# Performance work log

Hardware: AMD Instinct MI355X
Metric: run time of the kernel (lower is better)

Reference implementation:

```python
import jax, jax.numpy as jnp
import numpy as np

# Grid / filter configuration (matches init_kwargs)
NLAT_IN, NLON_IN = 361, 720
NLAT_OUT, NLON_OUT = 361, 720
K = 9                       # kernel_size for piecewise-linear basis, kernel_shape=[3,4]
PSCALE = NLON_IN // NLON_OUT  # longitude stride between output longitudes
NNZ = 65536
B, CIN, COUT = 2, 64, 64


def setup_inputs() -> dict:
    key = jax.random.key(0)
    k0, k1, k2, k3, k4, k5 = jax.random.split(key, 6)
    x = jax.random.normal(k0, (B, CIN, NLAT_IN, NLON_IN), dtype=jnp.float32)
    psi_ker_idx = jax.random.randint(k1, (NNZ,), 0, K)
    psi_row_idx = jax.random.randint(k2, (NNZ,), 0, NLAT_OUT)
    psi_col_idx = jax.random.randint(k3, (NNZ,), 0, NLAT_IN * NLON_IN)
    # quadrature-merged, normalized basis values are small positive numbers
    psi_vals = jax.random.uniform(k4, (NNZ,), dtype=jnp.float32) / K
    scale = (1.0 / (CIN * K)) ** 0.5
    weight = scale * jax.random.normal(k5, (COUT, CIN, K), dtype=jnp.float32)
    bias = jnp.zeros((COUT,), dtype=jnp.float32)
    return {
        "x": x,
        "psi_vals": psi_vals,
        "weight": weight,
        "bias": bias,
        "psi_ker_idx": psi_ker_idx,
        "psi_row_idx": psi_row_idx,
        "psi_col_idx": psi_col_idx,
    }


def reference(x, psi_vals, weight, bias, psi_ker_idx, psi_row_idx, psi_col_idx):
    """DISCO S2 conv: y[b,c,k,lo,p] = sum_nz psi_vals * x[b,c,lat_in, (lon_in+p*PSCALE)%NLON_IN]
    restricted to nz with ker==k, row==lo; then channel mixing with weight (COUT,CIN,K) + bias.
    Matches torch fallback which rolls x by PSCALE per output longitude and does sparse bmm."""
    b, c, nlat_in, nlon_in = x.shape
    lat_in = psi_col_idx // nlon_in          # (nnz,)
    lon_in = psi_col_idx % nlon_in           # (nnz,)
    seg = psi_ker_idx * NLAT_OUT + psi_row_idx  # (nnz,) segment id over (K, nlat_out)
    xf = x.reshape(b * c, nlat_in, nlon_in)

    def step(carry, p):
        lon = (lon_in + p * PSCALE) % nlon_in        # rolled longitude index, (nnz,)
        g = xf[:, lat_in, lon]                       # (BC, nnz) gather
        contrib = (psi_vals * g).T                   # (nnz, BC)
        yk = jax.ops.segment_sum(contrib, seg, num_segments=K * NLAT_OUT)  # (K*nlat_out, BC)
        y = yk.reshape(K, NLAT_OUT, b, c)
        o = jnp.einsum("klbc,ock->bol", y, weight)   # (B, COUT, nlat_out)
        return carry, o

    _, ys = jax.lax.scan(step, None, jnp.arange(NLON_OUT))  # (nlon_out, B, COUT, nlat_out)
    out = jnp.moveaxis(ys, 0, -1)                            # (B, COUT, nlat_out, nlon_out)
    return out + bias[None, :, None, None]
```

## Files before the change

### kernel.cpp

```cpp
#include <hip/hip_runtime.h>

typedef unsigned int uint;
typedef unsigned short ushort;

#define NLAT 361
#define NLON 720
#define NNZT 65536
#define CIN 64
#define COUT 64
#define NK 9
#define PADL 784
#define ROWCAP 384
#define CKTOT 576
#define YPS 168
#define WTS 640

typedef __attribute__((ext_vector_type(8))) short short8v;
typedef __attribute__((ext_vector_type(4))) float f32x4;

__device__ __forceinline__ float bfu(uint u){ return __uint_as_float(u<<16); }
__device__ __forceinline__ float bfh(uint u){ return __uint_as_float(u & 0xffff0000u); }
__device__ __forceinline__ ushort f2bf(float f){
  uint b = __float_as_uint(f);
  return (ushort)((b + 0x7fffu + ((b>>16)&1u)) >> 16);
}
__device__ __forceinline__ uint packbf2(float f0, float f1){
  uint b0 = __float_as_uint(f0), b1 = __float_as_uint(f1);
  uint r0 = (b0 + 0x7fffu + ((b0>>16)&1u)) >> 16;
  uint r1 = ((b1 + 0x7fffu + ((b1>>16)&1u)) >> 16) << 16;
  return r0 | r1;
}

__global__ __launch_bounds__(256) void k_csr(const int* __restrict__ ker, const int* __restrict__ row,
                                             const int* __restrict__ col, const float* __restrict__ vals,
                                             int2* __restrict__ meta_g, int* __restrict__ kptr_g){
  const int lo = blockIdx.x, tid = threadIdx.x;
  __shared__ int cnt2[256*NK];
  #pragma unroll
  for (int kk=0;kk<NK;kk++) cnt2[tid*NK+kk]=0;
  __syncthreads();
  for (int i=tid;i<NNZT;i+=256) if (row[i]==lo) cnt2[tid*NK + ker[i]]++;
  __syncthreads();
  if (tid==0){
    int run=0;
    for (int kk=0;kk<NK;kk++){
      kptr_g[lo*10+kk]=run;
      for (int t=0;t<256;t++){ int tmp=cnt2[t*NK+kk]; cnt2[t*NK+kk]=run; run+=tmp; }
    }
    kptr_g[lo*10+9]=run;
  }
  __syncthreads();
  for (int i=tid;i<NNZT;i+=256) if (row[i]==lo){
    int kk=ker[i];
    int off=cnt2[tid*NK+kk]++;
    if (off<ROWCAP){
      int c=col[i];
      meta_g[lo*ROWCAP+off]=make_int2(((c/NLON)<<16)|(c%NLON), __float_as_int(vals[i]));
    }
  }
}

__global__ __launch_bounds__(256) void k_xb(const float* __restrict__ x, ushort* __restrict__ xb){
  const int bid=blockIdx.x, tid=threadIdx.x;
  const int b=bid/NLAT, lat=bid-b*NLAT;
  const float* xs = x + (size_t)b*CIN*NLAT*NLON + (size_t)lat*NLON;
  ushort* xd = xb + (size_t)(b*NLAT+lat)*16*PADL*4;
  const size_t S=(size_t)NLAT*NLON;
  for (int idx=tid; idx<16*PADL; idx+=256){
    int cq=idx/PADL, j=idx-cq*PADL;
    int jj = (j<NLON)? j : j-NLON;
    const float* xc = xs + (size_t)(cq*4)*S + jj;
    uint lo32 = packbf2(xc[0], xc[S]);
    uint hi32 = packbf2(xc[2*S], xc[3*S]);
    *(uint2*)(xd + (size_t)(cq*PADL + j)*4) = make_uint2(lo32, hi32);
  }
}

__global__ __launch_bounds__(256) void k_wt(const float* __restrict__ w, ushort* __restrict__ wt){
  int idx = blockIdx.x*256 + threadIdx.x;
  if (idx >= COUT*WTS) return;
  int oc = idx/WTS, ckl = idx-oc*WTS;
  int chunk = ckl/160, q = ckl-chunk*160;
  ushort v = 0;
  if (q < 144) v = f2bf(w[oc*CKTOT + chunk*144 + q]);
  wt[oc*WTS + ckl] = v;
}

template<int USE_XB>
__global__ __launch_bounds__(256,3) void k_main(const float* __restrict__ x, const ushort* __restrict__ xb,
    const int2* __restrict__ meta_g, const int* __restrict__ kptr_g,
    const ushort* __restrict__ wt, const float* __restrict__ bias, float* __restrict__ out){
  const int bid=blockIdx.x, tid=threadIdx.x;
  const int lo=bid/6; const int rem=bid-lo*6;
  const int b=rem/3, pq=rem-(rem/3)*3;

  __shared__ int2 meta[ROWCAP];
  __shared__ __align__(16) ushort Yp[64*YPS];

  int kp[10];
  #pragma unroll
  for (int kk=0;kk<10;kk++){ int v=kptr_g[lo*10+kk]; kp[kk]=v<ROWCAP?v:ROWCAP; }
  for (int i=tid;i<kp[9];i+=256) meta[i]=meta_g[lo*ROWCAP+i];
  for (int idx=tid; idx<64*8; idx+=256){
    int p=idx>>3, j=idx&7;
    *(uint*)((char*)Yp + p*(YPS*2) + 288 + j*4) = 0;
  }
  __syncthreads();

  const int lane=tid&63, wv=tid>>6;
  const int l15=lane&15, kg=lane>>4;
  const char* xb8 = (const char*)xb + (size_t)b*NLAT*16*PADL*8;
  const char* wtb = (const char*)wt + ((wv*16+l15)*WTS + kg*8)*2;
  const char* ypb = (const char*)Yp + l15*(YPS*2) + kg*16;

  float b4[4];
  #pragma unroll
  for (int r=0;r<4;r++) b4[r]=bias[wv*16 + kg*4 + r];

  f32x4 outacc[4][4];
  #pragma unroll
  for (int a=0;a<4;a++)
    #pragma unroll
    for (int c2=0;c2<4;c2++) outacc[a][c2]=(f32x4)0.f;

  for (int chunk=0;chunk<4;chunk++){
    const int c0=chunk*16;
    short8v af[5];
    #pragma unroll
    for (int ks=0;ks<5;ks++)
      af[ks] = *(const short8v*)(wtb + (chunk*160 + ks*32)*2);

    const uint cqoff = (uint)(chunk*4+wv)*(PADL*8);
    #pragma unroll
    for (int pt=0;pt<4;pt++){
      const int p0 = pq*240 + pt*64;
      float acc[4][NK];
      #pragma unroll
      for (int j=0;j<4;j++)
        #pragma unroll
        for (int kk=0;kk<NK;kk++) acc[j][kk]=0.f;

#define GBODY(M,KK) { \
      int lat=(M).x>>16, lon=(M).x&0xffff; \
      float v=__int_as_float((M).y); \
      int s=lon+p0; s=(s>=NLON)?s-NLON:s; \
      uint off=(uint)lat*(16u*PADL*8u)+cqoff+(uint)(s+lane)*8u; \
      uint2 u=*(const uint2*)(xb8+off); \
      acc[0][KK]+=v*bfu(u.x); acc[1][KK]+=v*bfh(u.x); \
      acc[2][KK]+=v*bfu(u.y); acc[3][KK]+=v*bfh(u.y); }

#define GBODYF(M,KK) { \
      int lat=(M).x>>16, lon=(M).x&0xffff; \
      float v=__int_as_float((M).y); \
      int s=lon+p0; s=(s>=NLON)?s-NLON:s; \
      int widx=s+lane; widx=(widx>=NLON)?widx-NLON:widx; \
      int base=((b*CIN + c0+wv*4)*NLAT + lat)*NLON + widx; \
      acc[0][KK]+=v*x[base]; \
      acc[1][KK]+=v*x[base+NLAT*NLON]; \
      acc[2][KK]+=v*x[base+2*NLAT*NLON]; \
      acc[3][KK]+=v*x[base+3*NLAT*NLON]; }

      #pragma unroll
      for (int kk=0;kk<NK;kk++){
        int i=kp[kk]; const int e=kp[kk+1];
        if (USE_XB){
          for (; i+3<e; i+=4){
            int2 m0=meta[i], m1=meta[i+1], m2=meta[i+2], m3=meta[i+3];
            GBODY(m0,kk); GBODY(m1,kk); GBODY(m2,kk); GBODY(m3,kk);
          }
          for (; i<e; i++){ int2 m0=meta[i]; GBODY(m0,kk); }
        } else {
          for (; i<e; i++){ int2 m0=meta[i]; GBODYF(m0,kk); }
        }
      }
#undef GBODY
#undef GBODYF
      __syncthreads();
      {
        char* dst = (char*)Yp + lane*(YPS*2) + wv*72;
        #pragma unroll
        for (int i2=0;i2<18;i2++){
          const int t0=2*i2, t1=2*i2+1;
          uint pr = packbf2(acc[t0/9][t0-9*(t0/9)], acc[t1/9][t1-9*(t1/9)]);
          *(uint*)(dst + i2*4) = pr;
        }
      }
      __syncthreads();
      #pragma unroll
      for (int ptile=0;ptile<4;ptile++){
        #pragma unroll
        for (int ks=0;ks<5;ks++){
          short8v bf = *(const short8v*)(ypb + ptile*(16*YPS*2) + ks*64);
          outacc[pt][ptile] = __builtin_amdgcn_mfma_f32_16x16x32_bf16(af[ks], bf, outacc[pt][ptile], 0, 0, 0);
        }
      }
    }
  }
  #pragma unroll
  for (int pt=0;pt<4;pt++)
    #pragma unroll
    for (int ptile=0;ptile<4;ptile++){
      const int pidx = pt*64 + ptile*16;
      if (pidx < 240){
        #pragma unroll
        for (int r=0;r<4;r++){
          int oc = wv*16 + kg*4 + r;
          int p  = pq*240 + pidx + l15;
          out[((size_t)(b*COUT+oc)*NLAT + lo)*NLON + p] = outacc[pt][ptile][r] + b4[r];
        }
      }
    }
}

extern "C" void kernel_launch(void* const* d_in, const int* in_sizes, int n_in,
                              void* d_out, int out_size, void* d_ws, size_t ws_size,
                              hipStream_t stream){
  const float* x   =(const float*)d_in[0];
  const float* vals=(const float*)d_in[1];
  const float* w   =(const float*)d_in[2];
  const float* bias=(const float*)d_in[3];
  const int* ker=(const int*)d_in[4];
  const int* row=(const int*)d_in[5];
  const int* col=(const int*)d_in[6];
  float* out=(float*)d_out;

  const size_t META_B=(size_t)NLAT*ROWCAP*sizeof(int2);
  const size_t KPTR_B=((size_t)NLAT*10*sizeof(int)+15)&~(size_t)15;
  const size_t WT_B=((size_t)COUT*WTS*sizeof(ushort)+15)&~(size_t)15;
  const size_t XB_B=(size_t)2*NLAT*16*PADL*4*sizeof(ushort);
  int2* meta_g=(int2*)d_ws;
  int*  kptr_g=(int*)((char*)d_ws+META_B);
  ushort* wt=(ushort*)((char*)d_ws+META_B+KPTR_B);
  ushort* xb=(ushort*)((char*)d_ws+META_B+KPTR_B+WT_B);
  const bool use_xb = ws_size >= META_B+KPTR_B+WT_B+XB_B;

  k_csr<<<dim3(NLAT), dim3(256), 0, stream>>>(ker,row,col,vals,meta_g,kptr_g);
  k_wt <<<dim3((COUT*WTS+255)/256), dim3(256), 0, stream>>>(w, wt);
  if (use_xb){
    k_xb<<<dim3(2*NLAT), dim3(256), 0, stream>>>(x, xb);
    k_main<1><<<dim3(NLAT*6), dim3(256), 0, stream>>>(x,xb,meta_g,kptr_g,wt,bias,out);
  } else {
    k_main<0><<<dim3(NLAT*6), dim3(256), 0, stream>>>(x,xb,meta_g,kptr_g,wt,bias,out);
  }
}
```

Baseline: 2.045 ms.

## Restructure DISCO main kernel: per-wave kernel-slot split, sorted nnz, cooperative grid sync

The main kernel is rebuilt so each block handles one (output latitude, batch) pair and covers all longitudes in three passes. Each wave now takes a balanced subset of the kernel-basis indices and accumulates 16 channels at once, instead of splitting channels across waves. The CSR build sorts nonzeros by gather address and packs value, kernel index and longitude into one word, with value precision truncated. A cooperative launch with grid-wide syncs keeps blocks in lockstep over channel chunks to improve L2 reuse of the bf16 input. The cost is grid-sync overhead, extra per-block setup work, and lower precision in psi values.

New measurement: 2.260 ms. 10.5% more time.

```diff
diff --git a/kernel.cpp b/kernel.cpp
--- a/kernel.cpp
+++ b/kernel.cpp
@@ -1,4 +1,5 @@
 #include <hip/hip_runtime.h>
+#include <hip/hip_cooperative_groups.h>
 
 typedef unsigned int uint;
 typedef unsigned short ushort;
@@ -14,6 +15,9 @@
 #define CKTOT 576
 #define YPS 168
 #define WTS 640
+#define XROWB (16*PADL*8)
+#define GRIDC 722
+#define OCAP 128
 
 typedef __attribute__((ext_vector_type(8))) short short8v;
 typedef __attribute__((ext_vector_type(4))) float f32x4;
@@ -35,29 +39,40 @@
                                              const int* __restrict__ col, const float* __restrict__ vals,
                                              int2* __restrict__ meta_g, int* __restrict__ kptr_g){
   const int lo = blockIdx.x, tid = threadIdx.x;
-  __shared__ int cnt2[256*NK];
-  #pragma unroll
-  for (int kk=0;kk<NK;kk++) cnt2[tid*NK+kk]=0;
-  __syncthreads();
-  for (int i=tid;i<NNZT;i+=256) if (row[i]==lo) cnt2[tid*NK + ker[i]]++;
-  __syncthreads();
-  if (tid==0){
-    int run=0;
-    for (int kk=0;kk<NK;kk++){
-      kptr_g[lo*10+kk]=run;
-      for (int t=0;t<256;t++){ int tmp=cnt2[t*NK+kk]; cnt2[t*NK+kk]=run; run+=tmp; }
-    }
-    kptr_g[lo*10+9]=run;
-  }
-  __syncthreads();
+  __shared__ int cnt[256];
+  __shared__ int2 list[ROWCAP];
+  __shared__ int kc[NK];
+  __shared__ int ntot;
+  int c=0;
+  for (int i=tid;i<NNZT;i+=256) if (row[i]==lo) c++;
+  cnt[tid]=c;
+  if (tid<NK) kc[tid]=0;
+  __syncthreads();
+  if (tid==0){ int run=0; for (int t=0;t<256;t++){ int tmp=cnt[t]; cnt[t]=run; run+=tmp; } ntot=run; }
+  __syncthreads();
+  int off=cnt[tid];
   for (int i=tid;i<NNZT;i+=256) if (row[i]==lo){
-    int kk=ker[i];
-    int off=cnt2[tid*NK+kk]++;
     if (off<ROWCAP){
-      int c=col[i];
-      meta_g[lo*ROWCAP+off]=make_int2(((c/NLON)<<16)|(c%NLON), __float_as_int(vals[i]));
-    }
-  }
+      int cc=col[i]; int lat=cc/NLON, lon=cc-lat*NLON;
+      int kk=ker[i];
+      uint vb=__float_as_uint(vals[i])&0xffffc000u;
+      list[off]=make_int2(lat*XROWB+lon*8, (int)(vb|((uint)kk<<10)|(uint)lon));
+      atomicAdd(&kc[kk],1);
+    }
+    off++;
+  }
+  __syncthreads();
+  int n = ntot; if (n>ROWCAP) n=ROWCAP;
+  for (int i=tid;i<n;i+=256){
+    uint xi=(uint)list[i].x; int r=0;
+    for (int j=0;j<n;j++){
+      uint xj=(uint)list[j].x;
+      r += (xj<xi) || (xj==xi && j<i);
+    }
+    meta_g[lo*ROWCAP+r]=list[i];
+  }
+  if (tid<NK) kptr_g[lo*10+tid]=kc[tid];
+  if (tid==NK) kptr_g[lo*10+9]=n;
 }
 
 __global__ __launch_bounds__(256) void k_xb(const float* __restrict__ x, ushort* __restrict__ xb){
@@ -82,134 +97,171 @@
   int oc = idx/WTS, ckl = idx-oc*WTS;
   int chunk = ckl/160, q = ckl-chunk*160;
   ushort v = 0;
-  if (q < 144) v = f2bf(w[oc*CKTOT + chunk*144 + q]);
+  if (q < 144){
+    int wvq=q/36, r=q-wvq*36;
+    int kk=r>>2, j=r&3;
+    v = f2bf(w[oc*CKTOT + (chunk*16 + wvq*4 + j)*NK + kk]);
+  }
   wt[oc*WTS + ckl] = v;
 }
 
-template<int USE_XB>
-__global__ __launch_bounds__(256,3) void k_main(const float* __restrict__ x, const ushort* __restrict__ xb,
+template<int USE_XB, int SYNC>
+__global__ __launch_bounds__(256,3) void k_coop(const float* __restrict__ x, const ushort* __restrict__ xb,
     const int2* __restrict__ meta_g, const int* __restrict__ kptr_g,
     const ushort* __restrict__ wt, const float* __restrict__ bias, float* __restrict__ out){
-  const int bid=blockIdx.x, tid=threadIdx.x;
-  const int lo=bid/6; const int rem=bid-lo*6;
-  const int b=rem/3, pq=rem-(rem/3)*3;
+  const int wid=blockIdx.x, tid=threadIdx.x;
+  const int lane=tid&63, wv=tid>>6, l15=lane&15, kg=lane>>4;
+  const int lo=wid>>1, b=wid&1;
 
   __shared__ int2 meta[ROWCAP];
   __shared__ __align__(16) ushort Yp[64*YPS];
-
-  int kp[10];
-  #pragma unroll
-  for (int kk=0;kk<10;kk++){ int v=kptr_g[lo*10+kk]; kp[kk]=v<ROWCAP?v:ROWCAP; }
-  for (int i=tid;i<kp[9];i+=256) meta[i]=meta_g[lo*ROWCAP+i];
+  __shared__ ushort olist[4*OCAP];
+
+  int n = kptr_g[lo*10+9]; if (n>ROWCAP) n=ROWCAP;
+  for (int i=tid;i<n;i+=256) meta[i]=meta_g[lo*ROWCAP+i];
+  int kbase, klen;
+  {
+    int P[10]; P[0]=0;
+    #pragma unroll
+    for (int k=0;k<9;k++) P[k+1]=P[k]+kptr_g[lo*10+k];
+    const int Bn[4][5]={{0,3,5,7,9},{0,2,5,7,9},{0,2,4,7,9},{0,2,4,6,9}};
+    int best=1<<30, br=0;
+    #pragma unroll
+    for (int r=0;r<4;r++){
+      int m0=P[Bn[r][1]]-P[0], m1=P[Bn[r][2]]-P[Bn[r][1]];
+      int m2=P[Bn[r][3]]-P[Bn[r][2]], m3=P[9]-P[Bn[r][3]];
+      int mx=max(max(m0,m1),max(m2,m3));
+      if (mx<best){best=mx;br=r;}
+    }
+    kbase=Bn[br][wv]; klen=Bn[br][wv+1]-Bn[br][wv];
+  }
   for (int idx=tid; idx<64*8; idx+=256){
     int p=idx>>3, j=idx&7;
-    *(uint*)((char*)Yp + p*(YPS*2) + 288 + j*4) = 0;
-  }
-  __syncthreads();
-
-  const int lane=tid&63, wv=tid>>6;
-  const int l15=lane&15, kg=lane>>4;
-  const char* xb8 = (const char*)xb + (size_t)b*NLAT*16*PADL*8;
+    *(uint*)((char*)Yp + p*(YPS*2) + 288 + j*4)=0;
+  }
+  __syncthreads();
+  int ocount=0;
+  for (int i=0;i<n;i++){
+    int k=(int)(((uint)meta[i].y>>10)&15u);
+    if ((unsigned)(k-kbase)<(unsigned)klen && ocount<OCAP){
+      if (lane==0) olist[wv*OCAP+ocount]=(ushort)i;
+      ocount++;
+    }
+  }
+  __syncthreads();
+
+  const char* xb8 = (const char*)xb + (size_t)b*NLAT*(size_t)XROWB;
   const char* wtb = (const char*)wt + ((wv*16+l15)*WTS + kg*8)*2;
   const char* ypb = (const char*)Yp + l15*(YPS*2) + kg*16;
-
-  float b4[4];
+  char* ydst = (char*)Yp + lane*(YPS*2);
+  const ushort* ol = &olist[wv*OCAP];
+  const int SS = NLAT*NLON;
+
+#define C16(S) { \
+  acc[0][0][S]+=v*bfu(u0.x); acc[0][1][S]+=v*bfh(u0.x); acc[0][2][S]+=v*bfu(u0.y); acc[0][3][S]+=v*bfh(u0.y); \
+  acc[1][0][S]+=v*bfu(u1.x); acc[1][1][S]+=v*bfh(u1.x); acc[1][2][S]+=v*bfu(u1.y); acc[1][3][S]+=v*bfh(u1.y); \
+  acc[2][0][S]+=v*bfu(u2.x); acc[2][1][S]+=v*bfh(u2.x); acc[2][2][S]+=v*bfu(u2.y); acc[2][3][S]+=v*bfh(u2.y); \
+  acc[3][0][S]+=v*bfu(u3.x); acc[3][1][S]+=v*bfh(u3.x); acc[3][2][S]+=v*bfu(u3.y); acc[3][3][S]+=v*bfh(u3.y); }
+#define C16F(S) { \
+  acc[0][0][S]+=v*x[fb]; acc[0][1][S]+=v*x[fb+SS]; acc[0][2][S]+=v*x[fb+2*SS]; acc[0][3][S]+=v*x[fb+3*SS]; \
+  acc[1][0][S]+=v*x[fb+4*SS]; acc[1][1][S]+=v*x[fb+5*SS]; acc[1][2][S]+=v*x[fb+6*SS]; acc[1][3][S]+=v*x[fb+7*SS]; \
+  acc[2][0][S]+=v*x[fb+8*SS]; acc[2][1][S]+=v*x[fb+9*SS]; acc[2][2][S]+=v*x[fb+10*SS]; acc[2][3][S]+=v*x[fb+11*SS]; \
+  acc[3][0][S]+=v*x[fb+12*SS]; acc[3][1][S]+=v*x[fb+13*SS]; acc[3][2][S]+=v*x[fb+14*SS]; acc[3][3][S]+=v*x[fb+15*SS]; }
+
+  f32x4 outacc[3][4];
   #pragma unroll
-  for (int r=0;r<4;r++) b4[r]=bias[wv*16 + kg*4 + r];
-
-  f32x4 outacc[4][4];
-  #pragma unroll
-  for (int a=0;a<4;a++)
+  for (int a=0;a<3;a++)
     #pragma unroll
     for (int c2=0;c2<4;c2++) outacc[a][c2]=(f32x4)0.f;
 
-  for (int chunk=0;chunk<4;chunk++){
-    const int c0=chunk*16;
-    short8v af[5];
-    #pragma unroll
-    for (int ks=0;ks<5;ks++)
-      af[ks] = *(const short8v*)(wtb + (chunk*160 + ks*32)*2);
-
-    const uint cqoff = (uint)(chunk*4+wv)*(PADL*8);
-    #pragma unroll
-    for (int pt=0;pt<4;pt++){
-      const int p0 = pq*240 + pt*64;
-      float acc[4][NK];
-      #pragma unroll
-      for (int j=0;j<4;j++)
+  for (int pt=0;pt<4;pt++){
+    for (int chunk=0;chunk<4;chunk++){
+      if constexpr (SYNC) cooperative_groups::this_grid().sync();
+      const char* xq0 = xb8 + (size_t)(chunk*4+0)*(PADL*8);
+      const char* xq1 = xb8 + (size_t)(chunk*4+1)*(PADL*8);
+      const char* xq2 = xb8 + (size_t)(chunk*4+2)*(PADL*8);
+      const char* xq3 = xb8 + (size_t)(chunk*4+3)*(PADL*8);
+      for (int it=0;it<3;it++){
+        const int p0 = it*240 + pt*64;
+        const uint thr = (uint)(NLON-p0);
+        const uint lanep8 = (uint)(lane+p0)*8u;
+        const bool act = (pt<3) || (lane<48);
+        const int jmax = act ? ocount : 0;
+        float acc[4][4][3];
         #pragma unroll
-        for (int kk=0;kk<NK;kk++) acc[j][kk]=0.f;
-
-#define GBODY(M,KK) { \
-      int lat=(M).x>>16, lon=(M).x&0xffff; \
-      float v=__int_as_float((M).y); \
-      int s=lon+p0; s=(s>=NLON)?s-NLON:s; \
-      uint off=(uint)lat*(16u*PADL*8u)+cqoff+(uint)(s+lane)*8u; \
-      uint2 u=*(const uint2*)(xb8+off); \
-      acc[0][KK]+=v*bfu(u.x); acc[1][KK]+=v*bfh(u.x); \
-      acc[2][KK]+=v*bfu(u.y); acc[3][KK]+=v*bfh(u.y); }
-
-#define GBODYF(M,KK) { \
-      int lat=(M).x>>16, lon=(M).x&0xffff; \
-      float v=__int_as_float((M).y); \
-      int s=lon+p0; s=(s>=NLON)?s-NLON:s; \
-      int widx=s+lane; widx=(widx>=NLON)?widx-NLON:widx; \
-      int base=((b*CIN + c0+wv*4)*NLAT + lat)*NLON + widx; \
-      acc[0][KK]+=v*x[base]; \
-      acc[1][KK]+=v*x[base+NLAT*NLON]; \
-      acc[2][KK]+=v*x[base+2*NLAT*NLON]; \
-      acc[3][KK]+=v*x[base+3*NLAT*NLON]; }
-
-      #pragma unroll
-      for (int kk=0;kk<NK;kk++){
-        int i=kp[kk]; const int e=kp[kk+1];
-        if (USE_XB){
-          for (; i+3<e; i+=4){
-            int2 m0=meta[i], m1=meta[i+1], m2=meta[i+2], m3=meta[i+3];
-            GBODY(m0,kk); GBODY(m1,kk); GBODY(m2,kk); GBODY(m3,kk);
+        for (int q=0;q<4;q++)
+          #pragma unroll
+          for (int j=0;j<4;j++)
+            #pragma unroll
+            for (int s=0;s<3;s++) acc[q][j][s]=0.f;
+
+        for (int j2=0;j2<jmax;j2++){
+          int i = ol[j2];
+          int2 m = meta[i];
+          uint ky = (uint)m.y;
+          int slot = (int)((ky>>10)&15u) - kbase;
+          float v = __uint_as_float(ky & 0xffffc000u);
+          if (USE_XB){
+            uint common = (uint)m.x + lanep8 + (((ky&0x3ffu) >= thr) ? (uint)-5760 : 0u);
+            uint2 u0=*(const uint2*)(xq0+common);
+            uint2 u1=*(const uint2*)(xq1+common);
+            uint2 u2=*(const uint2*)(xq2+common);
+            uint2 u3=*(const uint2*)(xq3+common);
+            if (slot==0){ C16(0) } else if (slot==1){ C16(1) } else { C16(2) }
+          } else {
+            int lat=(int)(((uint)m.x)/(uint)XROWB);
+            int s=(int)(ky&0x3ffu)+p0; s=(s>=NLON)?s-NLON:s;
+            int widx=s+lane; widx=(widx>=NLON)?widx-NLON:widx;
+            int fb=((b*CIN + chunk*16)*NLAT + lat)*NLON + widx;
+            if (slot==0){ C16F(0) } else if (slot==1){ C16F(1) } else { C16F(2) }
           }
-          for (; i<e; i++){ int2 m0=meta[i]; GBODY(m0,kk); }
-        } else {
-          for (; i<e; i++){ int2 m0=meta[i]; GBODYF(m0,kk); }
+        }
+        __syncthreads();
+        if (act){
+          #pragma unroll
+          for (int s=0;s<3;s++){
+            if (s<klen){
+              int kk=kbase+s;
+              #pragma unroll
+              for (int q=0;q<4;q++){
+                uint lo32=packbf2(acc[q][0][s],acc[q][1][s]);
+                uint hi32=packbf2(acc[q][2][s],acc[q][3][s]);
+                *(uint2*)(ydst + (q*36+kk*4)*2)=make_uint2(lo32,hi32);
+              }
+            }
+          }
+        }
+        __syncthreads();
+        #pragma unroll
+        for (int ptile=0;ptile<4;ptile++){
+          #pragma unroll
+          for (int ks=0;ks<5;ks++){
+            short8v bf = *(const short8v*)(ypb + ptile*(16*YPS*2) + ks*64);
+            short8v afk = *(const short8v*)(wtb + (chunk*160 + ks*32)*2);
+            outacc[it][ptile]=__builtin_amdgcn_mfma_f32_16x16x32_bf16(afk,bf,outacc[it][ptile],0,0,0);
+          }
         }
       }
-#undef GBODY
-#undef GBODYF
-      __syncthreads();
-      {
-        char* dst = (char*)Yp + lane*(YPS*2) + wv*72;
-        #pragma unroll
-        for (int i2=0;i2<18;i2++){
-          const int t0=2*i2, t1=2*i2+1;
-          uint pr = packbf2(acc[t0/9][t0-9*(t0/9)], acc[t1/9][t1-9*(t1/9)]);
-          *(uint*)(dst + i2*4) = pr;
-        }
-      }
-      __syncthreads();
+    }
+    #pragma unroll
+    for (int it=0;it<3;it++){
       #pragma unroll
       for (int ptile=0;ptile<4;ptile++){
-        #pragma unroll
-        for (int ks=0;ks<5;ks++){
-          short8v bf = *(const short8v*)(ypb + ptile*(16*YPS*2) + ks*64);
-          outacc[pt][ptile] = __builtin_amdgcn_mfma_f32_16x16x32_bf16(af[ks], bf, outacc[pt][ptile], 0, 0, 0);
+        const int pidx = pt*64 + ptile*16;
+        if (pidx < 240){
+          #pragma unroll
+          for (int r=0;r<4;r++){
+            int oc = wv*16 + kg*4 + r;
+            out[((size_t)(b*COUT+oc)*NLAT + lo)*NLON + it*240 + pidx + l15]
+              = outacc[it][ptile][r] + bias[oc];
+          }
         }
+        outacc[it][ptile]=(f32x4)0.f;
       }
     }
   }
-  #pragma unroll
-  for (int pt=0;pt<4;pt++)
-    #pragma unroll
-    for (int ptile=0;ptile<4;ptile++){
-      const int pidx = pt*64 + ptile*16;
-      if (pidx < 240){
-        #pragma unroll
-        for (int r=0;r<4;r++){
-          int oc = wv*16 + kg*4 + r;
-          int p  = pq*240 + pidx + l15;
-          out[((size_t)(b*COUT+oc)*NLAT + lo)*NLON + p] = outacc[pt][ptile][r] + b4[r];
-        }
-      }
-    }
+#undef C16
+#undef C16F
 }
 
 extern "C" void kernel_launch(void* const* d_in, const int* in_sizes, int n_in,
@@ -222,7 +274,7 @@
   const int* ker=(const int*)d_in[4];
   const int* row=(const int*)d_in[5];
   const int* col=(const int*)d_in[6];
-  float* out=(float*)d_out;
+  float* outp=(float*)d_out;
 
   const size_t META_B=(size_t)NLAT*ROWCAP*sizeof(int2);
   const size_t KPTR_B=((size_t)NLAT*10*sizeof(int)+15)&~(size_t)15;
@@ -236,10 +288,30 @@
 
   k_csr<<<dim3(NLAT), dim3(256), 0, stream>>>(ker,row,col,vals,meta_g,kptr_g);
   k_wt <<<dim3((COUT*WTS+255)/256), dim3(256), 0, stream>>>(w, wt);
-  if (use_xb){
+  if (use_xb)
     k_xb<<<dim3(2*NLAT), dim3(256), 0, stream>>>(x, xb);
-    k_main<1><<<dim3(NLAT*6), dim3(256), 0, stream>>>(x,xb,meta_g,kptr_g,wt,bias,out);
-  } else {
-    k_main<0><<<dim3(NLAT*6), dim3(256), 0, stream>>>(x,xb,meta_g,kptr_g,wt,bias,out);
-  }
-}
+
+  int dev=0; (void)hipGetDevice(&dev);
+  int coopAttr=0; (void)hipDeviceGetAttribute(&coopAttr, hipDeviceAttributeCooperativeLaunch, dev);
+  int ncu=0; (void)hipDeviceGetAttribute(&ncu, hipDeviceAttributeMultiprocessorCount, dev);
+
+  typedef void (*KFn)(const float*, const ushort*, const int2*, const int*,
+                      const ushort*, const float*, float*);
+  KFn fsync = use_xb ? (KFn)&k_coop<1,1> : (KFn)&k_coop<0,1>;
+  int nb=0;
+  (void)hipOccupancyMaxActiveBlocksPerMultiprocessor(&nb, fsync, 256, 0);
+
+  bool coop = (coopAttr!=0) && ((long)nb*(long)ncu >= (long)GRIDC);
+  if (coop){
+    const ushort* xbc = xb; const ushort* wtc = wt;
+    const int2* mgc = meta_g; const int* kpc = kptr_g;
+    void* params[7] = {(void*)&x,(void*)&xbc,(void*)&mgc,(void*)&kpc,(void*)&wtc,(void*)&bias,(void*)&outp};
+    hipError_t e = hipLaunchCooperativeKernel(reinterpret_cast<const void*>(fsync),
+                                              dim3(GRIDC), dim3(256), params, 0, stream);
+    if (e != hipSuccess){ (void)hipGetLastError(); coop=false; }
+  }
+  if (!coop){
+    if (use_xb) k_coop<1,0><<<dim3(GRIDC), dim3(256), 0, stream>>>(x,xb,meta_g,kptr_g,wt,bias,outp);
+    else        k_coop<0,0><<<dim3(GRIDC), dim3(256), 0, stream>>>(x,xb,meta_g,kptr_g,wt,bias,outp);
+  }
+}
```
